# Kernel optimization log

Measured on AMD Instinct MI355X. Metric: run time of the kernel, lower is better.

## Reference

```python
import jax, jax.numpy as jnp
import numpy as np
import math

B, N, H, C = 1, 2048, 8, 128
PQ, PV, R, CS, CZ = 8, 12, 2, 256, 128
CZ4 = CZ // 4
INF = 1e5
EPS = 1e-8
SOFTPLUS_INV_1 = 0.541324854612918


def _quat_to_rot(q):
    q = q / jnp.linalg.norm(q, axis=-1, keepdims=True)
    w, x, y, z = q[..., 0], q[..., 1], q[..., 2], q[..., 3]
    return jnp.stack([
        jnp.stack([1 - 2 * (y * y + z * z), 2 * (x * y - z * w), 2 * (x * z + y * w)], -1),
        jnp.stack([2 * (x * y + z * w), 1 - 2 * (x * x + z * z), 2 * (y * z - x * w)], -1),
        jnp.stack([2 * (x * z - y * w), 2 * (y * z + x * w), 1 - 2 * (x * x + y * y)], -1),
    ], -2)


def setup_inputs() -> dict:
    key = jax.random.key(0)
    ks = jax.random.split(key, 16)
    rn = lambda k, shape, s=1.0: jax.random.normal(k, shape, dtype=jnp.float32) * s
    hc = H * C
    return dict(
        s=rn(ks[0], (B, N, CS)),
        z_factor_1=rn(ks[1], (B, N, R, CZ)),
        z_factor_2=rn(ks[2], (B, N, R, CZ)),
        rot=_quat_to_rot(rn(ks[3], (B, N, 4))),
        trans=rn(ks[4], (B, N, 3)),
        mask=jnp.ones((B, N), dtype=bool),
        w_q=rn(ks[5], (hc, CS), 0.02), b_q=jnp.zeros((hc,), jnp.float32),
        w_kv=rn(ks[6], (2 * hc, CS), 0.02), b_kv=jnp.zeros((2 * hc,), jnp.float32),
        w_qp=rn(ks[7], (H * PQ * 3, CS), 0.02), b_qp=jnp.zeros((H * PQ * 3,), jnp.float32),
        w_kvp=rn(ks[8], (H * (PQ + PV) * 3, CS), 0.02), b_kvp=jnp.zeros((H * (PQ + PV) * 3,), jnp.float32),
        w_b=rn(ks[9], (H, CZ), 0.02), b_b=jnp.zeros((H,), jnp.float32),
        w_dz=rn(ks[10], (CZ4, CZ), 0.02), b_dz=jnp.zeros((CZ4,), jnp.float32),
        head_weights=jnp.full((H,), SOFTPLUS_INV_1, dtype=jnp.float32),
        w_out=rn(ks[11], (CS, H * (CZ4 + C + 4 * PV)), 0.02), b_out=jnp.zeros((CS,), jnp.float32),
    )


def _lin(x, w, b):
    return x @ w.T + b


def _ipa(s, z1, z2, rot, trans, mask, w_q, b_q, w_kv, b_kv, w_qp, b_qp,
         w_kvp, b_kvp, w_b, b_b, w_dz, b_dz, head_weights, w_out, b_out):
    q = _lin(s, w_q, b_q).reshape(B, N, H, C)
    kv = _lin(s, w_kv, b_kv).reshape(B, N, H, 2 * C)
    k, v = kv[..., :C], kv[..., C:]
    # local points -> global frame: x_glob = R x_loc + t
    qp = _lin(s, w_qp, b_qp).reshape(B, N, H * PQ, 3)
    qp = (jnp.einsum('bnij,bnpj->bnpi', rot, qp) + trans[:, :, None, :]).reshape(B, N, H, PQ, 3)
    kvp = _lin(s, w_kvp, b_kvp).reshape(B, N, H * (PQ + PV), 3)
    kvp = (jnp.einsum('bnij,bnpj->bnpi', rot, kvp) + trans[:, :, None, :]).reshape(B, N, H, PQ + PV, 3)
    kp, vp = kvp[..., :PQ, :], kvp[..., PQ:, :]
    # head weights: softplus init to 1, AF2 scaling sqrt(1/(3*(PQ*9/2)))
    hw = jax.nn.softplus(head_weights) * math.sqrt(1.0 / (3 * (PQ * 9.0 / 2)))
    # low-rank pair bias factors
    b1 = _lin(z1, w_b, b_b)   # [B,N,R,H]
    b2 = _lin(z2, w_b, b_b)
    z1d = _lin(z1, w_dz, b_dz)  # [B,N,R,CZ4]
    z2d = _lin(z2, w_dz, b_dz)
    # logits: scalar QK + point-distance + low-rank pair bias
    scalar = jnp.einsum('bihc,bjhc->bhij', q, k) * math.sqrt(1.0 / (3 * C))
    ptdot = jnp.einsum('bihpx,bjhpx->bhij', qp, kp)
    qn = jnp.sum(qp * qp, axis=(-1, -2))  # [B,N,H]
    kn = jnp.sum(kp * kp, axis=(-1, -2))
    pt_term = hw[None, :, None, None] * (
        ptdot - 0.5 * qn.transpose(0, 2, 1)[:, :, :, None] - 0.5 * kn.transpose(0, 2, 1)[:, :, None, :])
    pair = jnp.einsum('birh,bjrh->bhij', b1, b2)
    mask_bias = jnp.where(mask, 0.0, -INF)[:, None, None, :]
    a = jax.nn.softmax(scalar + pt_term + pair + mask_bias, axis=-1)  # [B,H,N,N]
    # outputs
    o = jnp.einsum('bhij,bjhc->bihc', a, v).reshape(B, N, H * C)
    opt = jnp.einsum('bhij,bjhpx->bihpx', a, vp)  # global-frame points
    opt_loc = jnp.einsum('bnji,bnhpj->bnhpi', rot, opt - trans[:, :, None, None, :])  # R^T (x - t)
    opt_norm = jnp.sqrt(jnp.sum(opt_loc * opt_loc, axis=-1) + EPS)  # [B,N,H,PV]
    oz = jnp.einsum('bhij,bjrc->bihrc', a, z2d)
    opair = jnp.sum(oz * z1d[:, :, None, :, :], axis=3)  # [B,N,H,CZ4]
    feats = jnp.concatenate([
        o,
        opt_loc[..., 0].reshape(B, N, H * PV),
        opt_loc[..., 1].reshape(B, N, H * PV),
        opt_loc[..., 2].reshape(B, N, H * PV),
        opt_norm.reshape(B, N, H * PV),
        opair.reshape(B, N, H * CZ4),
    ], axis=-1)
    return _lin(feats, w_out, b_out)  # [B,N,CS]


def reference(s, z_factor_1, z_factor_2, rot, trans, mask, w_q, b_q, w_kv, b_kv,
              w_qp, b_qp, w_kvp, b_kvp, w_b, b_b, w_dz, b_dz, head_weights,
              w_out, b_out):
    return _ipa(s, z_factor_1, z_factor_2, rot, trans, mask, w_q, b_q, w_kv, b_kv,
                w_qp, b_qp, w_kvp, b_kvp, w_b, b_b, w_dz, b_dz, head_weights,
                w_out, b_out)
```

## Files before the change

kernel.cpp:

```cpp
#include <hip/hip_runtime.h>
#include <math.h>

#define NN   2048
#define HH   8
#define CC   128
#define PQn  8
#define PVn  12
#define RRn  2
#define CSn  256
#define CZn  128
#define CZ4n 32
#define HC   (HH*CC)
#define FEAT (HC + 4*HH*PVn + HH*CZ4n)
#define DA   160
#define DVP  256
#define DVU  240
#define QKV  3840
#define LOG2E 1.4426950408889634f

typedef unsigned short ushort_t;
#define AS1 __attribute__((address_space(1)))
#define AS3 __attribute__((address_space(3)))

using bfrag = __attribute__((ext_vector_type(8))) short;
using ffrag = __attribute__((ext_vector_type(4))) float;

__device__ inline ushort_t f2bf(float x) {
    union { float f; unsigned int u; } v; v.f = x;
    unsigned int r = v.u + 0x7fffu + ((v.u >> 16) & 1u);
    return (ushort_t)(r >> 16);
}
__device__ inline float bf2f(ushort_t x) {
    union { unsigned int u; float f; } v; v.u = ((unsigned int)x) << 16; return v.f;
}

struct CvtArgs {
    const float4* src[12];
    ushort4* dst[12];
    int n4[12];
};
__global__ __launch_bounds__(256) void cvtn_kernel(CvtArgs a,
    float4* __restrict__ outp, const float4* __restrict__ bias4)
{
    int i = blockIdx.x * 256 + threadIdx.x;
    if (i < NN * CSn / 4) {
        outp[i] = bias4[i & 63];
        return;
    }
    i -= NN * CSn / 4;
#pragma unroll
    for (int k = 0; k < 12; ++k) {
        if (i < a.n4[k]) {
            ushort4 o;
            if (a.src[k]) {
                float4 v = a.src[k][i];
                o = make_ushort4(f2bf(v.x), f2bf(v.y), f2bf(v.z), f2bf(v.w));
            } else {
                o = make_ushort4(0, 0, 0, 0);
            }
            a.dst[k][i] = o;
            return;
        }
        i -= a.n4[k];
    }
}

__global__ __launch_bounds__(256) void bgemm_kernel(
    const ushort_t* __restrict__ A, size_t sA,
    const ushort_t* __restrict__ B, size_t sB,
    void* __restrict__ Cv, size_t sC,
    const float* __restrict__ bias, size_t sBias,
    int ldk, int kOff, int kOffPerZ, int kLen, int ldc, int obf, int atomicOut)
{
    const int z = blockIdx.z;
    A += (size_t)z * sA;
    B += (size_t)z * sB;
    const float* bp = bias ? (bias + (size_t)z * sBias) : nullptr;
    const int k0beg = kOff + z * kOffPerZ;
    const int r0 = blockIdx.y * 128;
    const int c0 = blockIdx.x * 128;
    __shared__ __align__(16) ushort_t lA[128 * 32];
    __shared__ __align__(16) ushort_t lB[128 * 32];
    const int tid = threadIdx.x;
    const int w = tid >> 6, lane = tid & 63;
    const int wm = (w >> 1) * 64, wn = (w & 1) * 64;
    const int lrA = lane >> 2;
    const int lcA = (lane & 3) * 8;
    ffrag acc[4][4] = {};

    for (int k0 = k0beg; k0 < k0beg + kLen; k0 += 32) {
#pragma unroll
        for (int t = 0; t < 2; ++t) {
            int instr = w * 2 + t;
            int r = instr * 16 + lrA;
            const ushort_t* ga = A + (size_t)(r0 + r) * ldk + k0 + lcA;
            const ushort_t* gb = B + (size_t)(c0 + r) * ldk + k0 + lcA;
            __builtin_amdgcn_global_load_lds((const AS1 void*)ga,
                (AS3 void*)((AS3 ushort_t*)&lA[instr * 512 + lane * 8]), 16, 0, 0);
            __builtin_amdgcn_global_load_lds((const AS1 void*)gb,
                (AS3 void*)((AS3 ushort_t*)&lB[instr * 512 + lane * 8]), 16, 0, 0);
        }
        __syncthreads();
        bfrag af[4], bf[4];
#pragma unroll
        for (int mi = 0; mi < 4; ++mi)
            af[mi] = *(const bfrag*)&lA[(wm + mi * 16 + (lane & 15)) * 32 + (lane >> 4) * 8];
#pragma unroll
        for (int ni = 0; ni < 4; ++ni)
            bf[ni] = *(const bfrag*)&lB[(wn + ni * 16 + (lane & 15)) * 32 + (lane >> 4) * 8];
#pragma unroll
        for (int mi = 0; mi < 4; ++mi)
#pragma unroll
            for (int ni = 0; ni < 4; ++ni)
                acc[mi][ni] = __builtin_amdgcn_mfma_f32_16x16x32_bf16(af[mi], bf[ni], acc[mi][ni], 0, 0, 0);
        __syncthreads();
    }
#pragma unroll
    for (int mi = 0; mi < 4; ++mi) {
#pragma unroll
        for (int ni = 0; ni < 4; ++ni) {
            int col = c0 + wn + ni * 16 + (lane & 15);
            float bv = bp ? bp[col] : 0.f;
#pragma unroll
            for (int rr = 0; rr < 4; ++rr) {
                int row = r0 + wm + mi * 16 + (lane >> 4) * 4 + rr;
                float val = acc[mi][ni][rr] + bv;
                if (atomicOut)
                    unsafeAtomicAdd(&((float*)Cv)[(size_t)z * sC + (size_t)row * ldc + col], val);
                else if (obf)
                    ((ushort_t*)Cv)[(size_t)z * sC + (size_t)row * ldc + col] = f2bf(val);
                else
                    ((float*)Cv)[(size_t)z * sC + (size_t)row * ldc + col] = val;
            }
        }
    }
}

__global__ __launch_bounds__(256) void mgemm_kernel(
    const ushort_t* __restrict__ A0, const ushort_t* __restrict__ B0,
    ushort_t* __restrict__ C0,
    const ushort_t* __restrict__ A1, const ushort_t* __restrict__ B1,
    ushort_t* __restrict__ C1)
{
    const int bx = blockIdx.x;
    const ushort_t *A, *B;
    ushort_t* C;
    int ldk, kLen, ldc, r0, c0;
    if (bx < 480) {
        A = A0; B = B0; C = C0;
        ldk = CSn; kLen = CSn; ldc = QKV;
        r0 = (bx / 30) * 128;
        c0 = (bx % 30) * 128;
    } else {
        int i = bx - 480;
        A = A1; B = B1; C = C1;
        ldk = CZn; kLen = CZn; ldc = 128;
        r0 = i * 128;
        c0 = 0;
    }
    __shared__ __align__(16) ushort_t lA[128 * 32];
    __shared__ __align__(16) ushort_t lB[128 * 32];
    const int tid = threadIdx.x;
    const int w = tid >> 6, lane = tid & 63;
    const int wm = (w >> 1) * 64, wn = (w & 1) * 64;
    const int lrA = lane >> 2;
    const int lcA = (lane & 3) * 8;
    ffrag acc[4][4] = {};

    for (int k0 = 0; k0 < kLen; k0 += 32) {
#pragma unroll
        for (int t = 0; t < 2; ++t) {
            int instr = w * 2 + t;
            int r = instr * 16 + lrA;
            const ushort_t* ga = A + (size_t)(r0 + r) * ldk + k0 + lcA;
            const ushort_t* gb = B + (size_t)(c0 + r) * ldk + k0 + lcA;
            __builtin_amdgcn_global_load_lds((const AS1 void*)ga,
                (AS3 void*)((AS3 ushort_t*)&lA[instr * 512 + lane * 8]), 16, 0, 0);
            __builtin_amdgcn_global_load_lds((const AS1 void*)gb,
                (AS3 void*)((AS3 ushort_t*)&lB[instr * 512 + lane * 8]), 16, 0, 0);
        }
        __syncthreads();
        bfrag af[4], bf[4];
#pragma unroll
        for (int mi = 0; mi < 4; ++mi)
            af[mi] = *(const bfrag*)&lA[(wm + mi * 16 + (lane & 15)) * 32 + (lane >> 4) * 8];
#pragma unroll
        for (int ni = 0; ni < 4; ++ni)
            bf[ni] = *(const bfrag*)&lB[(wn + ni * 16 + (lane & 15)) * 32 + (lane >> 4) * 8];
#pragma unroll
        for (int mi = 0; mi < 4; ++mi)
#pragma unroll
            for (int ni = 0; ni < 4; ++ni)
                acc[mi][ni] = __builtin_amdgcn_mfma_f32_16x16x32_bf16(af[mi], bf[ni], acc[mi][ni], 0, 0, 0);
        __syncthreads();
    }
#pragma unroll
    for (int mi = 0; mi < 4; ++mi) {
#pragma unroll
        for (int ni = 0; ni < 4; ++ni) {
            int col = c0 + wn + ni * 16 + (lane & 15);
#pragma unroll
            for (int rr = 0; rr < 4; ++rr) {
                int row = r0 + wm + mi * 16 + (lane >> 4) * 4 + rr;
                C[(size_t)row * ldc + col] = f2bf(acc[mi][ni][rr]);
            }
        }
    }
}

__global__ __launch_bounds__(256) void prep_kernel(
    const ushort_t* __restrict__ qkv,
    const ushort_t* __restrict__ zproj,
    const float* __restrict__ b_q, const float* __restrict__ b_kv,
    const float* __restrict__ b_qp, const float* __restrict__ b_kvp,
    const float* __restrict__ b_b, const float* __restrict__ b_dz,
    const float* __restrict__ rot, const float* __restrict__ trans,
    const float* __restrict__ hwts,
    ushort_t* __restrict__ qaug, ushort_t* __restrict__ kaug,
    ushort_t* __restrict__ vaug)
{
    const int i = blockIdx.x;
    const int tid = threadIdx.x;
    __shared__ float R[9], t[3];
    __shared__ float qp_l[192], kp_l[192], vp_l[288];
    __shared__ float kn_s[8], hw_s[8];
    __shared__ __align__(16) ushort_t qa_s[8 * DA];
    __shared__ __align__(16) ushort_t ka_s[8 * DA];
    __shared__ __align__(16) ushort_t va_s[8 * DVP];
    if (tid < 9) R[tid] = rot[i*9 + tid];
    if (tid < 3) t[tid] = trans[i*3 + tid];
    if (tid < 8) {
        hw_s[tid] = log1pf(expf(hwts[tid])) * 0.09622504486493763f;
        kn_s[tid] = 0.f;
    }
    __syncthreads();
    if (tid < 64) {
        const ushort_t* v = qkv + (size_t)i*QKV + 3072 + tid*3;
        float vx = bf2f(v[0]) + b_qp[tid*3+0];
        float vy = bf2f(v[1]) + b_qp[tid*3+1];
        float vz = bf2f(v[2]) + b_qp[tid*3+2];
        float X = R[0]*vx + R[1]*vy + R[2]*vz + t[0];
        float Y = R[3]*vx + R[4]*vy + R[5]*vz + t[1];
        float Z = R[6]*vx + R[7]*vy + R[8]*vz + t[2];
        qp_l[tid*3+0] = X; qp_l[tid*3+1] = Y; qp_l[tid*3+2] = Z;
    } else if (tid < 224) {
        int p = tid - 64;
        int h = p / 20, pp = p % 20;
        const ushort_t* v = qkv + (size_t)i*QKV + 3264 + p*3;
        float vx = bf2f(v[0]) + b_kvp[p*3+0];
        float vy = bf2f(v[1]) + b_kvp[p*3+1];
        float vz = bf2f(v[2]) + b_kvp[p*3+2];
        float X = R[0]*vx + R[1]*vy + R[2]*vz + t[0];
        float Y = R[3]*vx + R[4]*vy + R[5]*vz + t[1];
        float Z = R[6]*vx + R[7]*vy + R[8]*vz + t[2];
        if (pp < 8) {
            int b = (h*8 + pp) * 3;
            kp_l[b+0] = X; kp_l[b+1] = Y; kp_l[b+2] = Z;
            atomicAdd(&kn_s[h], X*X + Y*Y + Z*Z);
        } else {
            int b = (h*12 + pp - 8) * 3;
            vp_l[b+0] = X; vp_l[b+1] = Y; vp_l[b+2] = Z;
        }
    }
    __syncthreads();

    const float QS = 0.05103103630798288f * LOG2E;
    if (tid < 128) {
        int h = tid >> 4, d = (tid & 15) * 8;
        bfrag q8 = *(const bfrag*)(qkv + (size_t)i*QKV + h*128 + d);
        bfrag k8 = *(const bfrag*)(qkv + (size_t)i*QKV + 1024 + h*256 + d);
        ushort_t qo[8], ko[8];
#pragma unroll
        for (int e = 0; e < 8; ++e) {
            qo[e] = f2bf(QS * (bf2f((ushort_t)q8[e]) + b_q[h*128 + d + e]));
            ko[e] = f2bf(bf2f((ushort_t)k8[e]) + b_kv[h*256 + d + e]);
        }
        *(bfrag*)&qa_s[h*DA + d] = *(bfrag*)qo;
        *(bfrag*)&ka_s[h*DA + d] = *(bfrag*)ko;
    }
    {
        int h = tid >> 5, d = 128 + (tid & 31);
        float qv, kv2;
        if (d < 152) {
            qv  = hw_s[h] * LOG2E * qp_l[h*24 + d - 128];
            kv2 = kp_l[h*24 + d - 128];
        } else if (d < 154) {
            int r = d - 152;
            qv  = LOG2E * (bf2f(zproj[(size_t)(i*2 + r)*128 + h]) + b_b[h]);
            kv2 = bf2f(zproj[(size_t)(4096 + i*2 + r)*128 + h]) + b_b[h];
        } else if (d == 154) {
            qv  = LOG2E;
            kv2 = -0.5f * hw_s[h] * kn_s[h];
        } else { qv = 0.f; kv2 = 0.f; }
        qa_s[h*DA + d] = f2bf(qv);
        ka_s[h*DA + d] = f2bf(kv2);
    }
    if (tid < 128) {
        int h = tid >> 4, d = (tid & 15) * 8;
        bfrag v8 = *(const bfrag*)(qkv + (size_t)i*QKV + 1024 + h*256 + 128 + d);
        ushort_t vo[8];
#pragma unroll
        for (int e = 0; e < 8; ++e)
            vo[e] = f2bf(bf2f((ushort_t)v8[e]) + b_kv[h*256 + 128 + d + e]);
        *(bfrag*)&va_s[h*DVP + d] = *(bfrag*)vo;
    }
#pragma unroll
    for (int k = 0; k < 4; ++k) {
        int idx = k * 256 + tid;
        int h = idx >> 7, d = 128 + (idx & 127);
        float v;
        if (d < 164)       v = vp_l[h*36 + d - 128];
        else if (d < 196)  v = bf2f(zproj[(size_t)(4096 + i*2 + 0)*128 + 8 + d - 164]) + b_dz[d - 164];
        else if (d < 228)  v = bf2f(zproj[(size_t)(4096 + i*2 + 1)*128 + 8 + d - 196]) + b_dz[d - 196];
        else if (d == 239) v = 1.0f;
        else               v = 0.f;
        va_s[h*DVP + d] = f2bf(v);
    }
    __syncthreads();

    for (int idx = tid; idx < 576; idx += 256) {
        if (idx < 160) {
            int h = idx / 20, dg = (idx - h*20) * 8;
            *(bfrag*)(qaug + ((size_t)h*NN + i) * DA + dg) = *(const bfrag*)&qa_s[h*DA + dg];
        } else if (idx < 320) {
            int r = idx - 160;
            int h = r / 20, dg = (r - h*20) * 8;
            *(bfrag*)(kaug + ((size_t)h*NN + i) * DA + dg) = *(const bfrag*)&ka_s[h*DA + dg];
        } else {
            int r = idx - 320;
            int h = r >> 5, dg = (r & 31) * 8;
            *(bfrag*)(vaug + ((size_t)h*NN + i) * DVP + dg) = *(const bfrag*)&va_s[h*DVP + dg];
        }
    }
}

__global__ __launch_bounds__(256) void transpose_kernel(
    const ushort_t* __restrict__ in, ushort_t* __restrict__ out)
{
    const int z = blockIdx.z;
    in  += (size_t)z * NN * DVP;
    out += (size_t)z * NN * DVP;
    const int i0 = blockIdx.x * 64;
    const int d0 = blockIdx.y * 64;
    __shared__ __align__(8) ushort_t tb[64][72];
    const int tid = threadIdx.x;
#pragma unroll
    for (int p = 0; p < 4; ++p) {
        int idx = p * 256 + tid;
        int r = idx >> 4, sg = idx & 15;
        ushort4 v = *(const ushort4*)(in + (size_t)(i0 + r) * DVP + d0 + sg * 4);
        *(ushort4*)&tb[r][sg * 4] = v;
    }
    __syncthreads();
#pragma unroll
    for (int p = 0; p < 4; ++p) {
        int idx = p * 256 + tid;
        int d = idx >> 4, ig = idx & 15;
        ushort4 v = make_ushort4(tb[ig*4+0][d], tb[ig*4+1][d],
                                 tb[ig*4+2][d], tb[ig*4+3][d]);
        *(ushort4*)(out + (size_t)(d0 + d) * NN + i0 + ig * 4) = v;
    }
}

__global__ __launch_bounds__(1024, 4) void flash_kernel(
    const ushort_t* __restrict__ qaug,
    const ushort_t* __restrict__ kaug,
    const ushort_t* __restrict__ vaugT,
    ushort_t* __restrict__ Opart,
    float* __restrict__ Lpart)
{
    const int bid = blockIdx.x;
    const int G = bid & 15;
    const int m = bid >> 4;
    const int h = G >> 1;
    const int g = G & 1;
    const int i0 = m * 128;

    __shared__ __align__(16) ushort_t Kt[2][64 * 168];
    __shared__ __align__(16) ushort_t Vt[2][DVU * 72];
    __shared__ __align__(16) ushort_t Pl[2][128 * 72];

    const int tid = threadIdx.x;
    const int w = tid >> 6, lane = tid & 63;
    const int quad = lane >> 4, lc = lane & 15;
    const int rq = w >> 1, jq = w & 1;
    const int rh = w >> 2, dh = (w >> 1) & 1, jc = w & 1;

    const ushort_t* qh = qaug + (size_t)h * NN * DA;
    const ushort_t* kh = kaug + (size_t)h * NN * DA;
    const ushort_t* vh = vaugT + (size_t)h * DVP * NN;

    const int j0g = g * 1024;
    const int iK0 = tid, iK1 = 1024 + tid;
    const int rK0 = iK0 / 21, oK0 = iK0 - rK0 * 21;
    const int rK1 = iK1 / 21, oK1 = iK1 - rK1 * 21;
    const bool vK1 = (tid < 320);
    const ushort_t* kS0 = kh + (size_t)(j0g + rK0) * DA + (oK0 < 20 ? oK0 * 8 : 0);
    const ushort_t* kS1 = kh + (size_t)(j0g + rK1) * DA + (oK1 < 20 ? oK1 * 8 : 0);
    const int iV0 = tid, iV1 = 1024 + tid, iV2 = 2048 + tid;
    const int rV0 = iV0 / 9, oV0 = iV0 - rV0 * 9;
    const int rV1 = iV1 / 9, oV1 = iV1 - rV1 * 9;
    const int rV2 = iV2 / 9, oV2 = iV2 - rV2 * 9;
    const bool vV2 = (tid < 112);
    const ushort_t* vS0 = vh + (size_t)rV0 * NN + j0g + (oV0 < 8 ? oV0 * 8 : 0);
    const ushort_t* vS1 = vh + (size_t)rV1 * NN + j0g + (oV1 < 8 ? oV1 * 8 : 0);
    const ushort_t* vS2 = vh + (size_t)(vV2 ? rV2 : 0) * NN + j0g + (oV2 < 8 ? oV2 * 8 : 0);

    auto stageK = [&](ushort_t* dst) {
        __builtin_amdgcn_global_load_lds((const AS1 void*)kS0,
            (AS3 void*)((AS3 ushort_t*)&dst[iK0 * 8]), 16, 0, 0);
        if (vK1)
            __builtin_amdgcn_global_load_lds((const AS1 void*)kS1,
                (AS3 void*)((AS3 ushort_t*)&dst[iK1 * 8]), 16, 0, 0);
        kS0 += 64 * DA; kS1 += 64 * DA;
    };
    auto stageV = [&](ushort_t* dst) {
        __builtin_amdgcn_global_load_lds((const AS1 void*)vS0,
            (AS3 void*)((AS3 ushort_t*)&dst[iV0 * 8]), 16, 0, 0);
        __builtin_amdgcn_global_load_lds((const AS1 void*)vS1,
            (AS3 void*)((AS3 ushort_t*)&dst[iV1 * 8]), 16, 0, 0);
        if (vV2)
            __builtin_amdgcn_global_load_lds((const AS1 void*)vS2,
                (AS3 void*)((AS3 ushort_t*)&dst[iV2 * 8]), 16, 0, 0);
        vS0 += 64; vS1 += 64; vS2 += 64;
    };

    bfrag qf[5];
#pragma unroll
    for (int ks = 0; ks < 5; ++ks)
        qf[ks] = *(const bfrag*)(qh + (size_t)(i0 + rq * 16 + lc) * DA + ks * 32 + quad * 8);

    ffrag acc[2][8];
#pragma unroll
    for (int mi = 0; mi < 2; ++mi)
#pragma unroll
        for (int t = 0; t < 8; ++t)
            acc[mi][t] = (ffrag){0.f, 0.f, 0.f, 0.f};

    stageK(Kt[0]);
    stageV(Vt[0]);
    __syncthreads();

    for (int it = 0; it < 16; ++it) {
        const int cur = it & 1;

        if (it < 15) stageK(Kt[cur ^ 1]);

        ffrag sf[2];
        sf[0] = (ffrag){0.f, 0.f, 0.f, 0.f};
        sf[1] = (ffrag){0.f, 0.f, 0.f, 0.f};
        const ushort_t* ktb = &Kt[cur][(jq * 32 + lc) * 168 + quad * 8];
        __builtin_amdgcn_s_setprio(1);
#pragma unroll
        for (int ks = 0; ks < 5; ++ks) {
            bfrag kf0 = *(const bfrag*)(ktb + ks * 32);
            bfrag kf1 = *(const bfrag*)(ktb + 16 * 168 + ks * 32);
            sf[0] = __builtin_amdgcn_mfma_f32_16x16x32_bf16(qf[ks], kf0, sf[0], 0, 0, 0);
            sf[1] = __builtin_amdgcn_mfma_f32_16x16x32_bf16(qf[ks], kf1, sf[1], 0, 0, 0);
        }

        if (it > 0) {
            const ushort_t* Plp = Pl[cur ^ 1];
            bfrag pf0 = *(const bfrag*)&Plp[(rh * 32 + lc) * 72 + jc * 32 + quad * 8];
            bfrag pf1 = *(const bfrag*)&Plp[(rh * 32 + 16 + lc) * 72 + jc * 32 + quad * 8];
            const ushort_t* vtb = &Vt[cur ^ 1][(dh * 128 + lc) * 72 + jc * 32 + quad * 8];
#pragma unroll
            for (int t = 0; t < 8; ++t) {
                if (dh && t == 7) continue;
                bfrag vf = *(const bfrag*)(vtb + t * 16 * 72);
                acc[0][t] = __builtin_amdgcn_mfma_f32_16x16x32_bf16(pf0, vf, acc[0][t], 0, 0, 0);
                acc[1][t] = __builtin_amdgcn_mfma_f32_16x16x32_bf16(pf1, vf, acc[1][t], 0, 0, 0);
            }
        }
        __builtin_amdgcn_s_setprio(0);

        {
            ushort_t* Plc = Pl[cur];
#pragma unroll
            for (int jt = 0; jt < 2; ++jt)
#pragma unroll
                for (int rr = 0; rr < 4; ++rr)
                    Plc[(rq * 16 + quad * 4 + rr) * 72 + jq * 32 + jt * 16 + lc] =
                        f2bf(exp2f(sf[jt][rr]));
        }

        __syncthreads();

        if (it < 15) stageV(Vt[cur ^ 1]);
    }

    {
        const ushort_t* Plp = Pl[1];
        bfrag pf0 = *(const bfrag*)&Plp[(rh * 32 + lc) * 72 + jc * 32 + quad * 8];
        bfrag pf1 = *(const bfrag*)&Plp[(rh * 32 + 16 + lc) * 72 + jc * 32 + quad * 8];
        const ushort_t* vtb = &Vt[1][(dh * 128 + lc) * 72 + jc * 32 + quad * 8];
#pragma unroll
        for (int t = 0; t < 8; ++t) {
            if (dh && t == 7) continue;
            bfrag vf = *(const bfrag*)(vtb + t * 16 * 72);
            acc[0][t] = __builtin_amdgcn_mfma_f32_16x16x32_bf16(pf0, vf, acc[0][t], 0, 0, 0);
            acc[1][t] = __builtin_amdgcn_mfma_f32_16x16x32_bf16(pf1, vf, acc[1][t], 0, 0, 0);
        }
    }

    ushort_t* scratch = (ushort_t*)Vt;
    const int pw = w >> 1;
    __syncthreads();
    if (jc == 1) {
        ushort_t tmp[64];
#pragma unroll
        for (int mi = 0; mi < 2; ++mi)
#pragma unroll
            for (int t = 0; t < 8; ++t)
#pragma unroll
                for (int rr = 0; rr < 4; ++rr)
                    tmp[mi*32 + t*4 + rr] = f2bf(acc[mi][t][rr]);
#pragma unroll
        for (int j = 0; j < 8; ++j)
            *(bfrag*)&scratch[pw * 4096 + j * 512 + lane * 8] = *(bfrag*)&tmp[j * 8];
    }
    __syncthreads();
    if (jc == 0) {
#pragma unroll
        for (int j = 0; j < 8; ++j) {
            bfrag v = *(const bfrag*)&scratch[pw * 4096 + j * 512 + lane * 8];
#pragma unroll
            for (int e = 0; e < 8; ++e) {
                int idx = j * 8 + e;
                acc[idx >> 5][(idx >> 2) & 7][idx & 3] += bf2f((ushort_t)v[e]);
            }
        }
        ushort_t* Ob = Opart + ((size_t)g * HH + h) * NN * DVU;
#pragma unroll
        for (int mi = 0; mi < 2; ++mi)
#pragma unroll
            for (int t = 0; t < 8; ++t) {
                if (dh && t == 7) continue;
                int dt = dh * 8 + t;
#pragma unroll
                for (int rr = 0; rr < 4; ++rr) {
                    int row = i0 + rh * 32 + mi * 16 + quad * 4 + rr;
                    Ob[(size_t)row * DVU + dt * 16 + lc] = f2bf(acc[mi][t][rr]);
                }
            }
        size_t sb = ((size_t)g * HH + h) * NN;
        if (dh == 1 && lc == 15) {
#pragma unroll
            for (int mi = 0; mi < 2; ++mi)
#pragma unroll
                for (int rr = 0; rr < 4; ++rr)
                    Lpart[sb + i0 + rh * 32 + mi * 16 + quad * 4 + rr] = acc[mi][6][rr];
        }
    }
}

__global__ __launch_bounds__(256) void combine_kernel(
    const ushort_t* __restrict__ Opart, const float* __restrict__ Lpart,
    const ushort_t* __restrict__ zproj, const float* __restrict__ b_dz,
    const float* __restrict__ rot, const float* __restrict__ trans,
    ushort_t* __restrict__ feats)
{
    const int i = blockIdx.x;
    const int tid = threadIdx.x;
    __shared__ float wgt8[8];
    __shared__ float Ol[8][DVU];
    if (tid < 8) {
        float l0 = Lpart[(size_t)(0 * HH + tid) * NN + i];
        float l1 = Lpart[(size_t)(1 * HH + tid) * NN + i];
        wgt8[tid] = 1.f / (l0 + l1);
    }
    __syncthreads();
    {
        int h = tid >> 5;
        int dg0 = tid & 31;
        for (int dg = dg0; dg < 60; dg += 32) {
            int d = dg * 4;
            ushort4 u0 = *(const ushort4*)&Opart[(((size_t)0 * HH + h) * NN + i) * DVU + d];
            ushort4 u1 = *(const ushort4*)&Opart[(((size_t)1 * HH + h) * NN + i) * DVU + d];
            float wv = wgt8[h];
            Ol[h][d+0] = (bf2f(u0.x) + bf2f(u1.x)) * wv;
            Ol[h][d+1] = (bf2f(u0.y) + bf2f(u1.y)) * wv;
            Ol[h][d+2] = (bf2f(u0.z) + bf2f(u1.z)) * wv;
            Ol[h][d+3] = (bf2f(u0.w) + bf2f(u1.w)) * wv;
        }
    }
    __syncthreads();

    ushort_t* f = feats + (size_t)i * FEAT;
    {
        int h = tid >> 5;
        int c = (tid * 4) & 127;
        ushort4 o4 = make_ushort4(f2bf(Ol[h][c]), f2bf(Ol[h][c+1]),
                                  f2bf(Ol[h][c+2]), f2bf(Ol[h][c+3]));
        *(ushort4*)(f + tid * 4) = o4;
    }
    if (tid < 96) {
        int h = tid / 12, p = tid % 12;
        const float* Rm = rot + i * 9;
        float ox = Ol[h][128 + p*3 + 0] - trans[i*3 + 0];
        float oy = Ol[h][128 + p*3 + 1] - trans[i*3 + 1];
        float oz = Ol[h][128 + p*3 + 2] - trans[i*3 + 2];
        float lx = Rm[0]*ox + Rm[3]*oy + Rm[6]*oz;
        float ly = Rm[1]*ox + Rm[4]*oy + Rm[7]*oz;
        float lz = Rm[2]*ox + Rm[5]*oy + Rm[8]*oz;
        float nrm = sqrtf(lx*lx + ly*ly + lz*lz + 1e-8f);
        f[1024 + 0*96 + tid] = f2bf(lx);
        f[1024 + 1*96 + tid] = f2bf(ly);
        f[1024 + 2*96 + tid] = f2bf(lz);
        f[1024 + 3*96 + tid] = f2bf(nrm);
    }
    {
        int h = tid >> 5, c = tid & 31;
        float z1d0 = bf2f(zproj[(size_t)(i*2 + 0)*128 + 8 + c]) + b_dz[c];
        float z1d1 = bf2f(zproj[(size_t)(i*2 + 1)*128 + 8 + c]) + b_dz[c];
        f[1408 + tid] = f2bf(Ol[h][164 + c] * z1d0 + Ol[h][196 + c] * z1d1);
    }
}

extern "C" void kernel_launch(void* const* d_in, const int* in_sizes, int n_in,
                              void* d_out, int out_size, void* d_ws, size_t ws_size,
                              hipStream_t stream) {
    const float* s     = (const float*)d_in[0];
    const float* z1    = (const float*)d_in[1];
    const float* z2    = (const float*)d_in[2];
    const float* rot   = (const float*)d_in[3];
    const float* trans = (const float*)d_in[4];
    const float* w_q   = (const float*)d_in[6];
    const float* b_q   = (const float*)d_in[7];
    const float* w_kv  = (const float*)d_in[8];
    const float* b_kv  = (const float*)d_in[9];
    const float* w_qp  = (const float*)d_in[10];
    const float* b_qp  = (const float*)d_in[11];
    const float* w_kvp = (const float*)d_in[12];
    const float* b_kvp = (const float*)d_in[13];
    const float* w_b   = (const float*)d_in[14];
    const float* b_b   = (const float*)d_in[15];
    const float* w_dz  = (const float*)d_in[16];
    const float* b_dz  = (const float*)d_in[17];
    const float* hwts  = (const float*)d_in[18];
    const float* w_out = (const float*)d_in[19];
    const float* b_out = (const float*)d_in[20];
    float* out = (float*)d_out;

    char* base = (char*)d_ws;
    const size_t OPART_BYTES = (size_t)4*HH*NN*DVU*2;
    char* S = base;
    ushort_t* s_bf  = (ushort_t*)(S);
    ushort_t* z_bf  = (ushort_t*)(S + 1048576);
    ushort_t* wall  = (ushort_t*)(S + 1048576 + 2097152);
    ushort_t* wz    = (ushort_t*)(S + 1048576 + 2097152 + 1966080);
    ushort_t* qkv   = (ushort_t*)(S + 1048576 + 2097152 + 1966080 + 32768);
    ushort_t* vaug  = (ushort_t*)(S + 1048576 + 2097152 + 1966080 + 32768 + 15728640);
    ushort_t* Opart = (ushort_t*)(S);
    char* P = base + OPART_BYTES;
    size_t off = 0;
    auto alloc = [&](size_t bytes) -> void* {
        void* p = P + off;
        off += (bytes + 255) & ~(size_t)255;
        return p;
    };
    ushort_t* wout_bf = (ushort_t*)alloc((size_t)CSn*FEAT*2);
    ushort_t* zproj   = (ushort_t*)alloc((size_t)8192*128*2);
    ushort_t* qaug    = (ushort_t*)alloc((size_t)HH*NN*DA*2);
    ushort_t* kaug    = (ushort_t*)alloc((size_t)HH*NN*DA*2);
    ushort_t* vaugT   = (ushort_t*)alloc((size_t)HH*NN*DVP*2);
    float*    Mpart   = (float*)alloc((size_t)4*HH*NN*4);
    float*    Lpart   = (float*)alloc((size_t)4*HH*NN*4);
    ushort_t* feats   = (ushort_t*)alloc((size_t)NN*FEAT*2);
    (void)Mpart;

    CvtArgs ca;
    int j = 0; int tot = 0;
    auto job = [&](const float* src, ushort_t* dst, int nElem) {
        ca.src[j] = (const float4*)src; ca.dst[j] = (ushort4*)dst; ca.n4[j] = nElem/4;
        tot += nElem/4; ++j;
    };
    job(s,     s_bf,              NN*CSn);
    job(z1,    z_bf,              4096*128);
    job(z2,    z_bf + 4096*128,   4096*128);
    job(w_q,   wall,              1024*256);
    job(w_kv,  wall + 1024*256,   2048*256);
    job(w_qp,  wall + 3072*256,   192*256);
    job(w_kvp, wall + 3264*256,   480*256);
    job(w_out, wout_bf,           CSn*FEAT);
    job(nullptr, wall + 3744*256, 96*256);
    job(w_b,   wz,                8*128);
    job(w_dz,  wz + 8*128,        32*128);
    job(nullptr, wz + 40*128,     88*128);
    tot += NN*CSn/4;
    cvtn_kernel<<<(tot + 255)/256, 256, 0, stream>>>(ca, (float4*)out, (const float4*)b_out);

    mgemm_kernel<<<544, 256, 0, stream>>>(s_bf, wall, qkv, z_bf, wz, zproj);

    prep_kernel<<<NN, 256, 0, stream>>>(qkv, zproj,
                                        b_q, b_kv, b_qp, b_kvp, b_b, b_dz,
                                        rot, trans, hwts, qaug, kaug, vaug);
    transpose_kernel<<<dim3(NN/64, DVP/64, HH), 256, 0, stream>>>(vaug, vaugT);

    flash_kernel<<<256, 1024, 0, stream>>>(
        qaug, kaug, vaugT, Opart, Lpart);

    combine_kernel<<<NN, 256, 0, stream>>>(Opart, Lpart, zproj, b_dz,
                                           rot, trans, feats);

    bgemm_kernel<<<dim3(CSn/128, NN/128, 4), 256, 0, stream>>>(
        feats, 0, wout_bf, 0, out, 0, nullptr, 0,
        FEAT, 0, FEAT/4, FEAT/4, CSn, 0, 1);
}
```

Measured before the change: 194.0 us.

## Fuse V transpose into prep kernel by tiling 64 rows per head

The prep kernel now processes a 64-row by one-head tile per block instead of one row across all heads. It writes the transposed V layout straight from shared memory, which removes the separate transpose kernel and the intermediate vaug buffer round trip. The cost is fewer blocks (256 instead of 2048), larger shared memory per block, and uncoalesced strided gathers from qkv within each tile.

```diff
diff --git a/kernel.cpp b/kernel.cpp
--- a/kernel.cpp
+++ b/kernel.cpp
@@ -217,148 +217,143 @@
     const float* __restrict__ rot, const float* __restrict__ trans,
     const float* __restrict__ hwts,
     ushort_t* __restrict__ qaug, ushort_t* __restrict__ kaug,
-    ushort_t* __restrict__ vaug)
+    ushort_t* __restrict__ vaugT)
 {
-    const int i = blockIdx.x;
+    const int b = blockIdx.x;
+    const int h = b & 7;
+    const int i0 = (b >> 3) * 64;
     const int tid = threadIdx.x;
-    __shared__ float R[9], t[3];
-    __shared__ float qp_l[192], kp_l[192], vp_l[288];
-    __shared__ float kn_s[8], hw_s[8];
-    __shared__ __align__(16) ushort_t qa_s[8 * DA];
-    __shared__ __align__(16) ushort_t ka_s[8 * DA];
-    __shared__ __align__(16) ushort_t va_s[8 * DVP];
-    if (tid < 9) R[tid] = rot[i*9 + tid];
-    if (tid < 3) t[tid] = trans[i*3 + tid];
-    if (tid < 8) {
-        hw_s[tid] = log1pf(expf(hwts[tid])) * 0.09622504486493763f;
-        kn_s[tid] = 0.f;
-    }
+
+    __shared__ float Rl[64][12];
+    __shared__ float kn_s[64];
+    __shared__ float qp_l[64 * 24];
+    __shared__ float kp_l[64 * 24];
+    __shared__ float vp_l[64 * 36];
+    __shared__ __align__(16) ushort_t qa_s[64 * 160];
+    __shared__ __align__(16) ushort_t ka_s[64 * 160];
+    __shared__ __align__(16) ushort_t va_s[64 * 264];
+
+    const float hw = log1pf(expf(hwts[h])) * 0.09622504486493763f;
+
+    for (int it = tid; it < 768; it += 256) {
+        int r = it / 12, c = it - r * 12;
+        Rl[r][c] = (c < 9) ? rot[(size_t)(i0 + r) * 9 + c]
+                           : trans[(size_t)(i0 + r) * 3 + (c - 9)];
+    }
+    if (tid < 64) kn_s[tid] = 0.f;
     __syncthreads();
-    if (tid < 64) {
-        const ushort_t* v = qkv + (size_t)i*QKV + 3072 + tid*3;
-        float vx = bf2f(v[0]) + b_qp[tid*3+0];
-        float vy = bf2f(v[1]) + b_qp[tid*3+1];
-        float vz = bf2f(v[2]) + b_qp[tid*3+2];
-        float X = R[0]*vx + R[1]*vy + R[2]*vz + t[0];
-        float Y = R[3]*vx + R[4]*vy + R[5]*vz + t[1];
-        float Z = R[6]*vx + R[7]*vy + R[8]*vz + t[2];
-        qp_l[tid*3+0] = X; qp_l[tid*3+1] = Y; qp_l[tid*3+2] = Z;
-    } else if (tid < 224) {
-        int p = tid - 64;
-        int h = p / 20, pp = p % 20;
-        const ushort_t* v = qkv + (size_t)i*QKV + 3264 + p*3;
-        float vx = bf2f(v[0]) + b_kvp[p*3+0];
-        float vy = bf2f(v[1]) + b_kvp[p*3+1];
-        float vz = bf2f(v[2]) + b_kvp[p*3+2];
-        float X = R[0]*vx + R[1]*vy + R[2]*vz + t[0];
-        float Y = R[3]*vx + R[4]*vy + R[5]*vz + t[1];
-        float Z = R[6]*vx + R[7]*vy + R[8]*vz + t[2];
+
+    for (int it = tid; it < 512; it += 256) {
+        int r = it >> 3, pp = it & 7;
+        int gp = h * 8 + pp;
+        const ushort_t* v = qkv + (size_t)(i0 + r) * QKV + 3072 + gp * 3;
+        float vx = bf2f(v[0]) + b_qp[gp * 3 + 0];
+        float vy = bf2f(v[1]) + b_qp[gp * 3 + 1];
+        float vz = bf2f(v[2]) + b_qp[gp * 3 + 2];
+        const float* R = Rl[r];
+        qp_l[r * 24 + pp * 3 + 0] = R[0] * vx + R[1] * vy + R[2] * vz + R[9];
+        qp_l[r * 24 + pp * 3 + 1] = R[3] * vx + R[4] * vy + R[5] * vz + R[10];
+        qp_l[r * 24 + pp * 3 + 2] = R[6] * vx + R[7] * vy + R[8] * vz + R[11];
+    }
+    for (int it = tid; it < 1280; it += 256) {
+        int r = it / 20, pp = it - r * 20;
+        int gp = h * 20 + pp;
+        const ushort_t* v = qkv + (size_t)(i0 + r) * QKV + 3264 + gp * 3;
+        float vx = bf2f(v[0]) + b_kvp[gp * 3 + 0];
+        float vy = bf2f(v[1]) + b_kvp[gp * 3 + 1];
+        float vz = bf2f(v[2]) + b_kvp[gp * 3 + 2];
+        const float* R = Rl[r];
+        float X = R[0] * vx + R[1] * vy + R[2] * vz + R[9];
+        float Y = R[3] * vx + R[4] * vy + R[5] * vz + R[10];
+        float Z = R[6] * vx + R[7] * vy + R[8] * vz + R[11];
         if (pp < 8) {
-            int b = (h*8 + pp) * 3;
-            kp_l[b+0] = X; kp_l[b+1] = Y; kp_l[b+2] = Z;
-            atomicAdd(&kn_s[h], X*X + Y*Y + Z*Z);
+            kp_l[r * 24 + pp * 3 + 0] = X;
+            kp_l[r * 24 + pp * 3 + 1] = Y;
+            kp_l[r * 24 + pp * 3 + 2] = Z;
+            atomicAdd(&kn_s[r], X * X + Y * Y + Z * Z);
         } else {
-            int b = (h*12 + pp - 8) * 3;
-            vp_l[b+0] = X; vp_l[b+1] = Y; vp_l[b+2] = Z;
+            int q = pp - 8;
+            vp_l[r * 36 + q * 3 + 0] = X;
+            vp_l[r * 36 + q * 3 + 1] = Y;
+            vp_l[r * 36 + q * 3 + 2] = Z;
         }
     }
     __syncthreads();
 
     const float QS = 0.05103103630798288f * LOG2E;
-    if (tid < 128) {
-        int h = tid >> 4, d = (tid & 15) * 8;
-        bfrag q8 = *(const bfrag*)(qkv + (size_t)i*QKV + h*128 + d);
-        bfrag k8 = *(const bfrag*)(qkv + (size_t)i*QKV + 1024 + h*256 + d);
+    for (int it = tid; it < 1024; it += 256) {
+        int r = it >> 4, d = (it & 15) * 8;
+        bfrag q8 = *(const bfrag*)(qkv + (size_t)(i0 + r) * QKV + h * 128 + d);
+        bfrag k8 = *(const bfrag*)(qkv + (size_t)(i0 + r) * QKV + 1024 + h * 256 + d);
         ushort_t qo[8], ko[8];
 #pragma unroll
         for (int e = 0; e < 8; ++e) {
-            qo[e] = f2bf(QS * (bf2f((ushort_t)q8[e]) + b_q[h*128 + d + e]));
-            ko[e] = f2bf(bf2f((ushort_t)k8[e]) + b_kv[h*256 + d + e]);
-        }
-        *(bfrag*)&qa_s[h*DA + d] = *(bfrag*)qo;
-        *(bfrag*)&ka_s[h*DA + d] = *(bfrag*)ko;
-    }
-    {
-        int h = tid >> 5, d = 128 + (tid & 31);
+            qo[e] = f2bf(QS * (bf2f((ushort_t)q8[e]) + b_q[h * 128 + d + e]));
+            ko[e] = f2bf(bf2f((ushort_t)k8[e]) + b_kv[h * 256 + d + e]);
+        }
+        *(bfrag*)&qa_s[r * 160 + d] = *(bfrag*)qo;
+        *(bfrag*)&ka_s[r * 160 + d] = *(bfrag*)ko;
+    }
+    for (int it = tid; it < 2048; it += 256) {
+        int r = it >> 5, d = 128 + (it & 31);
+        int i = i0 + r;
         float qv, kv2;
         if (d < 152) {
-            qv  = hw_s[h] * LOG2E * qp_l[h*24 + d - 128];
-            kv2 = kp_l[h*24 + d - 128];
+            qv  = hw * LOG2E * qp_l[r * 24 + d - 128];
+            kv2 = kp_l[r * 24 + d - 128];
         } else if (d < 154) {
-            int r = d - 152;
-            qv  = LOG2E * (bf2f(zproj[(size_t)(i*2 + r)*128 + h]) + b_b[h]);
-            kv2 = bf2f(zproj[(size_t)(4096 + i*2 + r)*128 + h]) + b_b[h];
+            int rz = d - 152;
+            qv  = LOG2E * (bf2f(zproj[(size_t)(i * 2 + rz) * 128 + h]) + b_b[h]);
+            kv2 = bf2f(zproj[(size_t)(4096 + i * 2 + rz) * 128 + h]) + b_b[h];
         } else if (d == 154) {
             qv  = LOG2E;
-            kv2 = -0.5f * hw_s[h] * kn_s[h];
+            kv2 = -0.5f * hw * kn_s[r];
         } else { qv = 0.f; kv2 = 0.f; }
-        qa_s[h*DA + d] = f2bf(qv);
-        ka_s[h*DA + d] = f2bf(kv2);
-    }
-    if (tid < 128) {
-        int h = tid >> 4, d = (tid & 15) * 8;
-        bfrag v8 = *(const bfrag*)(qkv + (size_t)i*QKV + 1024 + h*256 + 128 + d);
+        qa_s[r * 160 + d] = f2bf(qv);
+        ka_s[r * 160 + d] = f2bf(kv2);
+    }
+    for (int it = tid; it < 1024; it += 256) {
+        int r = it >> 4, d = (it & 15) * 8;
+        bfrag v8 = *(const bfrag*)(qkv + (size_t)(i0 + r) * QKV + 1024 + h * 256 + 128 + d);
         ushort_t vo[8];
 #pragma unroll
         for (int e = 0; e < 8; ++e)
-            vo[e] = f2bf(bf2f((ushort_t)v8[e]) + b_kv[h*256 + 128 + d + e]);
-        *(bfrag*)&va_s[h*DVP + d] = *(bfrag*)vo;
-    }
-#pragma unroll
-    for (int k = 0; k < 4; ++k) {
-        int idx = k * 256 + tid;
-        int h = idx >> 7, d = 128 + (idx & 127);
+            vo[e] = f2bf(bf2f((ushort_t)v8[e]) + b_kv[h * 256 + 128 + d + e]);
+        *(bfrag*)&va_s[r * 264 + d] = *(bfrag*)vo;
+    }
+    for (int it = tid; it < 8192; it += 256) {
+        int r = it >> 7, d = 128 + (it & 127);
+        int i = i0 + r;
         float v;
-        if (d < 164)       v = vp_l[h*36 + d - 128];
-        else if (d < 196)  v = bf2f(zproj[(size_t)(4096 + i*2 + 0)*128 + 8 + d - 164]) + b_dz[d - 164];
-        else if (d < 228)  v = bf2f(zproj[(size_t)(4096 + i*2 + 1)*128 + 8 + d - 196]) + b_dz[d - 196];
+        if (d < 164)       v = vp_l[r * 36 + d - 128];
+        else if (d < 196)  v = bf2f(zproj[(size_t)(4096 + i * 2 + 0) * 128 + 8 + d - 164]) + b_dz[d - 164];
+        else if (d < 228)  v = bf2f(zproj[(size_t)(4096 + i * 2 + 1) * 128 + 8 + d - 196]) + b_dz[d - 196];
         else if (d == 239) v = 1.0f;
         else               v = 0.f;
-        va_s[h*DVP + d] = f2bf(v);
+        va_s[r * 264 + d] = f2bf(v);
     }
     __syncthreads();
 
-    for (int idx = tid; idx < 576; idx += 256) {
-        if (idx < 160) {
-            int h = idx / 20, dg = (idx - h*20) * 8;
-            *(bfrag*)(qaug + ((size_t)h*NN + i) * DA + dg) = *(const bfrag*)&qa_s[h*DA + dg];
-        } else if (idx < 320) {
-            int r = idx - 160;
-            int h = r / 20, dg = (r - h*20) * 8;
-            *(bfrag*)(kaug + ((size_t)h*NN + i) * DA + dg) = *(const bfrag*)&ka_s[h*DA + dg];
+    for (int it = tid; it < 2560; it += 256) {
+        if (it < 1280) {
+            int r = it / 20, ch = it - r * 20;
+            *(bfrag*)(qaug + ((size_t)h * NN + i0 + r) * DA + ch * 8) =
+                *(const bfrag*)&qa_s[r * 160 + ch * 8];
         } else {
-            int r = idx - 320;
-            int h = r >> 5, dg = (r & 31) * 8;
-            *(bfrag*)(vaug + ((size_t)h*NN + i) * DVP + dg) = *(const bfrag*)&va_s[h*DVP + dg];
-        }
-    }
-}
-
-__global__ __launch_bounds__(256) void transpose_kernel(
-    const ushort_t* __restrict__ in, ushort_t* __restrict__ out)
-{
-    const int z = blockIdx.z;
-    in  += (size_t)z * NN * DVP;
-    out += (size_t)z * NN * DVP;
-    const int i0 = blockIdx.x * 64;
-    const int d0 = blockIdx.y * 64;
-    __shared__ __align__(8) ushort_t tb[64][72];
-    const int tid = threadIdx.x;
-#pragma unroll
-    for (int p = 0; p < 4; ++p) {
-        int idx = p * 256 + tid;
-        int r = idx >> 4, sg = idx & 15;
-        ushort4 v = *(const ushort4*)(in + (size_t)(i0 + r) * DVP + d0 + sg * 4);
-        *(ushort4*)&tb[r][sg * 4] = v;
-    }
-    __syncthreads();
-#pragma unroll
-    for (int p = 0; p < 4; ++p) {
-        int idx = p * 256 + tid;
-        int d = idx >> 4, ig = idx & 15;
-        ushort4 v = make_ushort4(tb[ig*4+0][d], tb[ig*4+1][d],
-                                 tb[ig*4+2][d], tb[ig*4+3][d]);
-        *(ushort4*)(out + (size_t)(d0 + d) * NN + i0 + ig * 4) = v;
+            int t2 = it - 1280;
+            int r = t2 / 20, ch = t2 - r * 20;
+            *(bfrag*)(kaug + ((size_t)h * NN + i0 + r) * DA + ch * 8) =
+                *(const bfrag*)&ka_s[r * 160 + ch * 8];
+        }
+    }
+    ushort_t* vT = vaugT + (size_t)h * DVP * NN;
+    for (int it = tid; it < 4096; it += 256) {
+        int d = it >> 4, ig = it & 15;
+        ushort4 v = make_ushort4(va_s[(ig * 4 + 0) * 264 + d],
+                                 va_s[(ig * 4 + 1) * 264 + d],
+                                 va_s[(ig * 4 + 2) * 264 + d],
+                                 va_s[(ig * 4 + 3) * 264 + d]);
+        *(ushort4*)(vT + (size_t)d * NN + i0 + ig * 4) = v;
     }
 }
 
@@ -514,7 +509,7 @@
             for (int t = 0; t < 8; ++t)
 #pragma unroll
                 for (int rr = 0; rr < 4; ++rr)
-                    tmp[mi*32 + t*4 + rr] = f2bf(acc[mi][t][rr]);
+                    tmp[mi * 32 + t * 4 + rr] = f2bf(acc[mi][t][rr]);
 #pragma unroll
         for (int j = 0; j < 8; ++j)
             *(bfrag*)&scratch[pw * 4096 + j * 512 + lane * 8] = *(bfrag*)&tmp[j * 8];
@@ -650,7 +645,6 @@
     ushort_t* wall  = (ushort_t*)(S + 1048576 + 2097152);
     ushort_t* wz    = (ushort_t*)(S + 1048576 + 2097152 + 1966080);
     ushort_t* qkv   = (ushort_t*)(S + 1048576 + 2097152 + 1966080 + 32768);
-    ushort_t* vaug  = (ushort_t*)(S + 1048576 + 2097152 + 1966080 + 32768 + 15728640);
     ushort_t* Opart = (ushort_t*)(S);
     char* P = base + OPART_BYTES;
     size_t off = 0;
@@ -692,10 +686,9 @@
 
     mgemm_kernel<<<544, 256, 0, stream>>>(s_bf, wall, qkv, z_bf, wz, zproj);
 
-    prep_kernel<<<NN, 256, 0, stream>>>(qkv, zproj,
-                                        b_q, b_kv, b_qp, b_kvp, b_b, b_dz,
-                                        rot, trans, hwts, qaug, kaug, vaug);
-    transpose_kernel<<<dim3(NN/64, DVP/64, HH), 256, 0, stream>>>(vaug, vaugT);
+    prep_kernel<<<256, 256, 0, stream>>>(qkv, zproj,
+                                         b_q, b_kv, b_qp, b_kvp, b_b, b_dz,
+                                         rot, trans, hwts, qaug, kaug, vaugT);
 
     flash_kernel<<<256, 1024, 0, stream>>>(
         qaug, kaug, vaugT, Opart, Lpart);
```

Measured after the change: 206.1 us. 1.06x slower.
